# Kernel tuning notes

Hardware: AMD Instinct MI355X
Metric: run time of the kernel (lower is better)

Reference implementation:

```python
import jax, jax.numpy as jnp
import numpy as np

B, C, H, W = 2, 3, 256, 256
K_STEPS = 50
RHO = 0.5
SIGMA_INIT = float(0.5 / np.sqrt(2.0 * C))  # sigma_init == tau_init = 0.5/sqrt(C*2)


def nabla(x):
    # forward finite differences, zero at last row/col. x: [B,C,H,W] -> [B,C,2,H,W]
    dh = jnp.pad(x[:, :, 1:, :] - x[:, :, :-1, :], ((0, 0), (0, 0), (0, 1), (0, 0)))
    dw = jnp.pad(x[:, :, :, 1:] - x[:, :, :, :-1], ((0, 0), (0, 0), (0, 0), (0, 1)))
    return jnp.stack([dh, dw], axis=2)


def nablaT(u):
    # adjoint of nabla (negative divergence). u: [B,C,2,H,W] -> [B,C,H,W]
    v0, v1 = u[:, :, 0], u[:, :, 1]
    out = jnp.zeros(v0.shape, v0.dtype)
    out = out.at[:, :, 1:, :].add(v0[:, :, :-1, :]).at[:, :, :-1, :].add(-v0[:, :, :-1, :])
    out = out.at[:, :, :, 1:].add(v1[:, :, :, :-1]).at[:, :, :, :-1].add(-v1[:, :, :, :-1])
    return out


def l12_prox_conjugate(v, lamb):
    # Moreau: prox_{sigma*(lamb*f)*}(v) = v - sigma*prox_{(lamb/sigma) f}(v/sigma)
    # which for L12 reduces to projection onto the lamb-ball per group.
    # groups: l2 over axes (1,-2,-1) = (C,H,W), one group per (B, F).
    norm = jnp.sqrt(jnp.sum(v * v, axis=(1, 3, 4), keepdims=True))
    scale = lamb / jnp.maximum(norm, lamb)  # == min(1, lamb/norm), safe at 0
    return v * scale


def l2_prox(z, y, gamma):
    # argmin_u 0.5||u-z||^2 + gamma*0.5||u-y||^2  (A = identity)
    return (z + gamma * y) / (1.0 + gamma)


def setup_inputs() -> dict:
    key = jax.random.key(0)
    y = jax.random.normal(key, (B, C, H, W), dtype=jnp.float32)
    lambd = jnp.float32(-1.0)  # learnable scalar log-regularization weight
    return {"y": y, "lambd": lambd}


def reference(y, lambd):
    elambda = jnp.exp(lambd)
    # set_init: A_dagger = identity
    x0 = y
    xt0 = jnp.zeros_like(x0)
    u0 = nabla(x0)

    def step(carry, _):
        x, xt, u, sigma, tau = carry
        u_next = l12_prox_conjugate(u + sigma * nabla(xt), elambda)
        x_next = l2_prox(x - tau * nablaT(u_next), y, tau)
        chi = 1.0 / jnp.sqrt(1.0 + 2.0 * RHO * tau)
        tau_next = tau * chi
        sigma_next = sigma / chi
        xt_next = (1.0 + chi) * x_next - chi * x
        return (x_next, xt_next, u_next, sigma_next, tau_next), None

    init = (x0, xt0, u0, jnp.float32(SIGMA_INIT), jnp.float32(SIGMA_INIT))
    (x, xt, u, _, _), _ = jax.lax.scan(step, init, None, length=K_STEPS)
    return (x, xt, u)
```

## Files before the change

kernel.cpp:

```cpp
#include <hip/hip_runtime.h>
#include <math.h>

constexpr int Cc = 3, Hh = 256;
constexpr int NX = 393216;
constexpr int R = 8;
constexpr int NBLK = 192;
constexpr int KSTEPS = 50;
constexpr int ROWQ = 128;
constexpr int BROWS = 12;
constexpr int SLOTQ = NBLK * BROWS * ROWQ;

using u64 = unsigned long long;
constexpr u64 SENT = 0x8000000080000000ull;

__device__ __forceinline__ float4 ld4(const float* p, int i) { return ((const float4*)p)[i]; }
__device__ __forceinline__ void st4(float* p, int i, float4 v) { ((float4*)p)[i] = v; }
__device__ __forceinline__ float4 mk4(float a, float b, float c, float d) { return make_float4(a, b, c, d); }
__device__ __forceinline__ u64 ldq(const u64* p) {
    return __hip_atomic_load(p, __ATOMIC_RELAXED, __HIP_MEMORY_SCOPE_AGENT);
}
__device__ __forceinline__ void stq(u64* p, u64 v) {
    __hip_atomic_store(p, v, __ATOMIC_RELAXED, __HIP_MEMORY_SCOPE_AGENT);
}
__device__ __forceinline__ void pub4(u64* w, float4 v) {
    union { float f[2]; u64 q; } a, b;
    a.f[0] = v.x; a.f[1] = v.y; b.f[0] = v.z; b.f[1] = v.w;
    stq(w, a.q); stq(w + 1, b.q);
}
__device__ __forceinline__ float4 unp(u64 lo, u64 hi) {
    union { u64 q; float f[2]; } a, b; a.q = lo; b.q = hi;
    return make_float4(a.f[0], a.f[1], b.f[0], b.f[1]);
}
__device__ __forceinline__ float4 col3(float4 P, float4 A, float4 B, float a, float b) {
    return mk4(fmaf(a, A.x, fmaf(b, B.x, P.x)), fmaf(a, A.y, fmaf(b, B.y, P.y)),
               fmaf(a, A.z, fmaf(b, B.z, P.z)), fmaf(a, A.w, fmaf(b, B.w, P.w)));
}
__device__ __forceinline__ float4 f4sub(float4 a, float4 b) {
    return mk4(a.x - b.x, a.y - b.y, a.z - b.z, a.w - b.w);
}
__device__ __forceinline__ float4 f4s(float4 a, float s) {
    return mk4(a.x * s, a.y * s, a.z * s, a.w * s);
}
__device__ __forceinline__ float4 f4fma(float s, float4 a, float4 b) {
    return mk4(fmaf(s, a.x, b.x), fmaf(s, a.y, b.y), fmaf(s, a.z, b.z), fmaf(s, a.w, b.w));
}
__device__ __forceinline__ float4 nth(float4 vm, bool up, float4 v0x, bool dn) {
    return mk4((up ? vm.x : 0.f) - (dn ? v0x.x : 0.f), (up ? vm.y : 0.f) - (dn ? v0x.y : 0.f),
               (up ? vm.z : 0.f) - (dn ? v0x.z : 0.f), (up ? vm.w : 0.f) - (dn ? v0x.w : 0.f));
}
__device__ __forceinline__ float4 ntw(float4 v1x, int c4) {
    float ul = __shfl_up(v1x.w, 1, 64);
    return mk4(((c4 > 0) ? ul : 0.f) - v1x.x, v1x.x - v1x.y, v1x.y - v1x.z,
               v1x.z - ((c4 < 63) ? v1x.w : 0.f));
}
__device__ __forceinline__ float4 gradw(float4 t, int c4) {
    float xn = __shfl_down(t.x, 1, 64);
    return mk4(t.y - t.x, t.z - t.y, t.w - t.z, (c4 < 63) ? (xn - t.w) : 0.f);
}
__device__ __forceinline__ void barld() {
    asm volatile("s_waitcnt lgkmcnt(0)" ::: "memory");
    __builtin_amdgcn_sched_barrier(0);
    __builtin_amdgcn_s_barrier();
    __builtin_amdgcn_sched_barrier(0);
}

__global__ void init_ws(u64* h0, u64* h1, u64* h2, u64* parts) {
    int i = blockIdx.x * 256 + threadIdx.x;
    if (i < SLOTQ) { h0[i] = SENT; h1[i] = SENT; h2[i] = SENT; }
    if (i < (KSTEPS + 1) * NBLK) parts[i] = SENT;
}

__global__ void __launch_bounds__(512, 1) cp_persist(
    const float* __restrict__ y, const float* __restrict__ lambd,
    float* __restrict__ xout, float* __restrict__ xtout, float* __restrict__ uout,
    u64* __restrict__ h0, u64* __restrict__ h1, u64* __restrict__ h2,
    u64* __restrict__ parts)
{
    __shared__ float sv0[8 * 256];
    __shared__ float sxtP[9 * 256];
    __shared__ float sxtA[9 * 256];
    __shared__ float sxtB[9 * 256];
    __shared__ float2 pw[8];

    const int tid = threadIdx.x, blk = blockIdx.x;
    const int bc = blk >> 5, tile = blk & 31, r0 = tile * R;
    const int c4 = tid & 63, trow = tid >> 6;
    const int b = (bc >= Cc) ? 1 : 0;
    const float lamb = expf(lambd[0]);
    const int gh = r0 + trow;
    const int j4 = bc * 16384 + gh * 64 + c4;

    float4 yv, xcur, v0c, v1c;
    float4 xpP, xpA, xpB, p0P, p0A, p0B, p1P, p1A, p1B;
    float4 yh = mk4(0, 0, 0, 0), vmtop = yh, v0h = yh, v1h = yh, xoh = yh;

    float tau = 0.20412414523193150818f;
    float sig = tau;
    float chi = 0.f, sigs = 0.f;
    float alpha = 0.f, beta = 0.f;

    auto slotp = [&](int r) -> u64* { return (r == 0) ? h0 : ((r == 1) ? h1 : h2); };

    auto wavesum2 = [&](float& a, float& bb) {
        #pragma unroll
        for (int m = 1; m < 64; m <<= 1) { a += __shfl_xor(a, m, 64); bb += __shfl_xor(bb, m, 64); }
    };

    auto pollscale = [&](int s) {
        const u64* pb = parts + (size_t)s * NBLK + b * 96;
        const int i1 = 64 + (c4 & 31);
        u64 q0, q1;
        for (;;) {
            q0 = ldq(pb + c4);
            q1 = ldq(pb + i1);
            if (__all((q0 != SENT) && (q1 != SENT))) break;
            __builtin_amdgcn_s_sleep(1);
        }
        asm volatile("" ::: "memory");
        union { u64 q; float f[2]; } a;
        a.q = q0;
        float g0 = a.f[0], g1 = a.f[1];
        a.q = q1;
        if (c4 < 32) { g0 += a.f[0]; g1 += a.f[1]; }
        wavesum2(g0, g1);
        alpha = lamb / fmaxf(sqrtf(g0), lamb);
        beta  = lamb / fmaxf(sqrtf(g1), lamb);
    };

    auto wavenorm = [&]() {
        float pa0 = v0c.x*v0c.x + v0c.y*v0c.y + v0c.z*v0c.z + v0c.w*v0c.w;
        float pa1 = v1c.x*v1c.x + v1c.y*v1c.y + v1c.z*v1c.z + v1c.w*v1c.w;
        wavesum2(pa0, pa1);
        if (c4 == 0) pw[trow] = make_float2(pa0, pa1);
    };
    auto pubparts = [&](int s) {
        if (tid == 0) {
            float q0 = 0.f, q1 = 0.f;
            #pragma unroll
            for (int w = 0; w < 8; ++w) { q0 += pw[w].x; q1 += pw[w].y; }
            union { float f[2]; u64 q; } pk; pk.f[0] = q0; pk.f[1] = q1;
            stq(parts + (size_t)s * NBLK + blk, pk.q);
        }
    };

    auto expand = [&](u64* hb, bool pub) {
        const float inv = 1.f / (1.f + tau);
        const float tin = tau * inv;
        const float opc = 1.f + chi;
        float4 xtP, xtA, xtB;
        {
            float4 vm = (trow > 0) ? ((float4*)(sv0 + (trow - 1) * 256))[c4] : vmtop;
            float4 NT0 = nth(vm, gh > 0, v0c, gh < Hh - 1);
            float4 NT1 = ntw(v1c, c4);
            float4 BASE = f4s(f4fma(tau, yv, xcur), inv);
            float4 xA = f4s(NT0, -tin);
            float4 xB = f4s(NT1, -tin);
            xpP = BASE; xpA = xA; xpB = xB;
            xtP = f4fma(-chi, xcur, f4s(BASE, opc));
            xtA = f4s(xA, opc);
            xtB = f4s(xB, opc);
            if (trow >= 1) {
                ((float4*)(sxtP + trow * 256))[c4] = xtP;
                ((float4*)(sxtA + trow * 256))[c4] = xtA;
                ((float4*)(sxtB + trow * 256))[c4] = xtB;
            }
            if (pub && trow == 0) {
                u64* rbase = hb + ((size_t)blk * BROWS) * ROWQ;
                pub4(rbase +  9 * ROWQ + 2 * c4, BASE);
                pub4(rbase + 10 * ROWQ + 2 * c4, xA);
                pub4(rbase + 11 * ROWQ + 2 * c4, xB);
            }
        }
        if (trow == 0 && tile < 31) {
            float4 vmh = ((float4*)(sv0 + 7 * 256))[c4];
            float4 NT0h = nth(vmh, true, v0h, true);
            float4 NT1h = ntw(v1h, c4);
            float4 BASEh = f4s(f4fma(tau, yh, xoh), inv);
            float4 xAh = f4s(NT0h, -tin);
            float4 xBh = f4s(NT1h, -tin);
            ((float4*)(sxtP + 8 * 256))[c4] = f4fma(-chi, xoh, f4s(BASEh, opc));
            ((float4*)(sxtA + 8 * 256))[c4] = f4s(xAh, opc);
            ((float4*)(sxtB + 8 * 256))[c4] = f4s(xBh, opc);
        }
        barld();
        {
            float4 dhP = mk4(0, 0, 0, 0), dhA = dhP, dhB = dhP;
            if (gh < Hh - 1) {
                dhP = f4sub(((float4*)(sxtP + (trow + 1) * 256))[c4], xtP);
                dhA = f4sub(((float4*)(sxtA + (trow + 1) * 256))[c4], xtA);
                dhB = f4sub(((float4*)(sxtB + (trow + 1) * 256))[c4], xtB);
            }
            float4 dwP = gradw(xtP, c4);
            float4 dwA = gradw(xtA, c4);
            float4 dwB = gradw(xtB, c4);
            p0P = f4s(dhP, sigs);
            p0A = f4fma(sigs, dhA, v0c);
            p0B = f4s(dhB, sigs);
            p1P = f4s(dwP, sigs);
            p1A = f4s(dwA, sigs);
            p1B = f4fma(sigs, dwB, v1c);
            if (pub) {
                u64* rbase = hb + ((size_t)blk * BROWS) * ROWQ;
                if (trow == 0) {
                    pub4(rbase + 3 * ROWQ + 2 * c4, p0P);
                    pub4(rbase + 4 * ROWQ + 2 * c4, p0A);
                    pub4(rbase + 5 * ROWQ + 2 * c4, p0B);
                    pub4(rbase + 6 * ROWQ + 2 * c4, p1P);
                    pub4(rbase + 7 * ROWQ + 2 * c4, p1A);
                    pub4(rbase + 8 * ROWQ + 2 * c4, p1B);
                }
                if (trow == 7) {
                    pub4(rbase + 0 * ROWQ + 2 * c4, p0P);
                    pub4(rbase + 1 * ROWQ + 2 * c4, p0A);
                    pub4(rbase + 2 * ROWQ + 2 * c4, p0B);
                }
            }
        }
        barld();
    };

    {
        yv = ld4(y, j4);
        xcur = yv;
        float4 dh = mk4(0, 0, 0, 0);
        if (gh < Hh - 1) dh = f4sub(ld4(y, j4 + 64), yv);
        v0c = dh;
        v1c = gradw(yv, c4);
        ((float4*)(sv0 + trow * 256))[c4] = v0c;
        if (trow == 0) {
            if (tile < 31) {
                const int j4h = bc * 16384 + (r0 + 8) * 64 + c4;
                yh = ld4(y, j4h);
                v0h = f4sub(ld4(y, j4h + 64), yh);
                v1h = gradw(yh, c4);
                xoh = yh;
            }
            if (tile > 0) {
                float4 ym = ld4(y, bc * 16384 + (r0 - 1) * 64 + c4);
                vmtop = f4sub(yv, ym);
            }
        }
        wavenorm();
        barld();
        pubparts(1);
        chi = 1.f / sqrtf(1.f + tau);
        sigs = sig / chi;
        expand(slotp(0), true);
        tau *= chi; sig = sigs;
    }

    for (int s = 1; s < KSTEPS; ++s) {
        pollscale(s);
        chi = 1.f / sqrtf(1.f + tau);
        sigs = sig / chi;

        xcur = col3(xpP, xpA, xpB, alpha, beta);
        v0c  = col3(p0P, p0A, p0B, alpha, beta);
        v1c  = col3(p1P, p1A, p1B, alpha, beta);
        ((float4*)(sv0 + trow * 256))[c4] = v0c;

        u64* hbp = slotp((s - 1) % 3);
        if (trow == 0) {
            if (tile > 0) {
                const u64* ra = hbp + ((size_t)(blk - 1) * BROWS) * ROWQ + 2 * c4;
                u64 a0, a1, a2, a3, a4, a5;
                for (;;) {
                    a0 = ldq(ra);            a1 = ldq(ra + 1);
                    a2 = ldq(ra + ROWQ);     a3 = ldq(ra + ROWQ + 1);
                    a4 = ldq(ra + 2 * ROWQ); a5 = ldq(ra + 2 * ROWQ + 1);
                    if (__all((a0 != SENT) && (a1 != SENT) && (a2 != SENT) &&
                              (a3 != SENT) && (a4 != SENT) && (a5 != SENT))) break;
                    __builtin_amdgcn_s_sleep(1);
                }
                vmtop = col3(unp(a0, a1), unp(a2, a3), unp(a4, a5), alpha, beta);
            }
            if (tile < 31) {
                const u64* rb = hbp + ((size_t)(blk + 1) * BROWS) * ROWQ + 2 * c4;
                u64 b0, b1, b2, b3, b4, b5, b6, b7, b8, b9, b10, b11, b12, b13, b14, b15, b16, b17;
                for (;;) {
                    b0  = ldq(rb + 3 * ROWQ);  b1  = ldq(rb + 3 * ROWQ + 1);
                    b2  = ldq(rb + 4 * ROWQ);  b3  = ldq(rb + 4 * ROWQ + 1);
                    b4  = ldq(rb + 5 * ROWQ);  b5  = ldq(rb + 5 * ROWQ + 1);
                    b6  = ldq(rb + 6 * ROWQ);  b7  = ldq(rb + 6 * ROWQ + 1);
                    b8  = ldq(rb + 7 * ROWQ);  b9  = ldq(rb + 7 * ROWQ + 1);
                    b10 = ldq(rb + 8 * ROWQ);  b11 = ldq(rb + 8 * ROWQ + 1);
                    b12 = ldq(rb + 9 * ROWQ);  b13 = ldq(rb + 9 * ROWQ + 1);
                    b14 = ldq(rb + 10 * ROWQ); b15 = ldq(rb + 10 * ROWQ + 1);
                    b16 = ldq(rb + 11 * ROWQ); b17 = ldq(rb + 11 * ROWQ + 1);
                    bool ok = (b0 != SENT) && (b1 != SENT) && (b2 != SENT) && (b3 != SENT) &&
                              (b4 != SENT) && (b5 != SENT) && (b6 != SENT) && (b7 != SENT) &&
                              (b8 != SENT) && (b9 != SENT) && (b10 != SENT) && (b11 != SENT) &&
                              (b12 != SENT) && (b13 != SENT) && (b14 != SENT) && (b15 != SENT) &&
                              (b16 != SENT) && (b17 != SENT);
                    if (__all(ok)) break;
                    __builtin_amdgcn_s_sleep(1);
                }
                v0h = col3(unp(b0, b1),   unp(b2, b3),   unp(b4, b5),   alpha, beta);
                v1h = col3(unp(b6, b7),   unp(b8, b9),   unp(b10, b11), alpha, beta);
                xoh = col3(unp(b12, b13), unp(b14, b15), unp(b16, b17), alpha, beta);
            }
        }
        asm volatile("" ::: "memory");

        if (s <= 47) {
            u64* rb2 = slotp((s + 1) % 3) + ((size_t)blk * BROWS) * ROWQ;
            if (trow == 0) {
                #pragma unroll
                for (int r = 3; r < 12; ++r) {
                    stq(rb2 + r * ROWQ + 2 * c4, SENT);
                    stq(rb2 + r * ROWQ + 2 * c4 + 1, SENT);
                }
            } else if (trow == 7) {
                #pragma unroll
                for (int r = 0; r < 3; ++r) {
                    stq(rb2 + r * ROWQ + 2 * c4, SENT);
                    stq(rb2 + r * ROWQ + 2 * c4 + 1, SENT);
                }
            }
        }
        wavenorm();
        barld();
        pubparts(s + 1);
        expand(slotp(s % 3), s < KSTEPS - 1);
        tau *= chi; sig = sigs;
    }

    pollscale(KSTEPS);
    const float opc = 1.f + chi;
    const int iv4 = bc * 32768 + gh * 64 + c4;
    float4 xf_ = col3(xpP, xpA, xpB, alpha, beta);
    float4 xtf = f4fma(-chi, xcur, f4s(xf_, opc));
    st4(xout, j4, xf_);
    st4(xtout, j4, xtf);
    st4(uout, iv4, f4s(v0c, alpha));
    st4(uout, iv4 + 16384, f4s(v1c, beta));
}

extern "C" void kernel_launch(void* const* d_in, const int* in_sizes, int n_in,
                              void* d_out, int out_size, void* d_ws, size_t ws_size,
                              hipStream_t stream) {
    (void)in_sizes; (void)n_in; (void)out_size; (void)ws_size;
    const float* y     = (const float*)d_in[0];
    const float* lambd = (const float*)d_in[1];
    float* xout  = (float*)d_out;
    float* xtout = xout + NX;
    float* uout  = xout + 2 * NX;

    u64* h0 = (u64*)d_out;
    u64* h1 = h0 + SLOTQ;
    u64* h2 = (u64*)d_ws;
    u64* parts = h2 + SLOTQ;

    init_ws<<<SLOTQ / 256, 256, 0, stream>>>(h0, h1, h2, parts);
    cp_persist<<<NBLK, 512, 0, stream>>>(y, lambd, xout, xtout, uout, h0, h1, h2, parts);
}
```

Baseline: 208.5 us.

## Publish per-wave norm partials and recompute neighbor rows to cut block barriers

Result: slower. 306.2 us (+46.9%).

```diff
diff --git a/kernel.cpp b/kernel.cpp
--- a/kernel.cpp
+++ b/kernel.cpp
@@ -9,6 +9,7 @@
 constexpr int ROWQ = 128;
 constexpr int BROWS = 12;
 constexpr int SLOTQ = NBLK * BROWS * ROWQ;
+constexpr int WPS = NBLK * 8;
 
 using u64 = unsigned long long;
 constexpr u64 SENT = 0x8000000080000000ull;
@@ -67,7 +68,7 @@
 __global__ void init_ws(u64* h0, u64* h1, u64* h2, u64* parts) {
     int i = blockIdx.x * 256 + threadIdx.x;
     if (i < SLOTQ) { h0[i] = SENT; h1[i] = SENT; h2[i] = SENT; }
-    if (i < (KSTEPS + 1) * NBLK) parts[i] = SENT;
+    if (i < (KSTEPS + 1) * WPS) parts[i] = SENT;
 }
 
 __global__ void __launch_bounds__(512, 1) cp_persist(
@@ -76,11 +77,8 @@
     u64* __restrict__ h0, u64* __restrict__ h1, u64* __restrict__ h2,
     u64* __restrict__ parts)
 {
-    __shared__ float sv0[8 * 256];
-    __shared__ float sxtP[9 * 256];
-    __shared__ float sxtA[9 * 256];
-    __shared__ float sxtB[9 * 256];
-    __shared__ float2 pw[8];
+    __shared__ float PCS[8][9][256];
+    __shared__ float sG[2];
 
     const int tid = threadIdx.x, blk = blockIdx.x;
     const int bc = blk >> 5, tile = blk & 31, r0 = tile * R;
@@ -89,180 +87,118 @@
     const float lamb = expf(lambd[0]);
     const int gh = r0 + trow;
     const int j4 = bc * 16384 + gh * 64 + c4;
-
-    float4 yv, xcur, v0c, v1c;
-    float4 xpP, xpA, xpB, p0P, p0A, p0B, p1P, p1A, p1B;
-    float4 yh = mk4(0, 0, 0, 0), vmtop = yh, v0h = yh, v1h = yh, xoh = yh;
-
-    float tau = 0.20412414523193150818f;
-    float sig = tau;
-    float chi = 0.f, sigs = 0.f;
-    float alpha = 0.f, beta = 0.f;
+    const bool have2 = (gh < Hh - 1);
+    const bool dn2 = (gh < Hh - 2);
+
+    float4 pc[9];
+    float4 xcur, x2, v0c, v0c2, v1c, v1c2, vm;
+    float4 yv, yv2;
+    float tau = 0.20412414523193150818f, sig = tau, chi, sigs;
 
     auto slotp = [&](int r) -> u64* { return (r == 0) ? h0 : ((r == 1) ? h1 : h2); };
-
+    auto ldsF = [&](int row, int f) -> float4& { return ((float4*)PCS[row][f])[c4]; };
     auto wavesum2 = [&](float& a, float& bb) {
         #pragma unroll
         for (int m = 1; m < 64; m <<= 1) { a += __shfl_xor(a, m, 64); bb += __shfl_xor(bb, m, 64); }
     };
-
-    auto pollscale = [&](int s) {
-        const u64* pb = parts + (size_t)s * NBLK + b * 96;
-        const int i1 = 64 + (c4 & 31);
-        u64 q0, q1;
+    auto pollparts = [&](int s, float& g0, float& g1) {
+        const u64* pb = parts + (size_t)s * WPS + b * 768 + c4 * 12;
+        u64 t[12];
         for (;;) {
-            q0 = ldq(pb + c4);
-            q1 = ldq(pb + i1);
-            if (__all((q0 != SENT) && (q1 != SENT))) break;
+            #pragma unroll
+            for (int i = 0; i < 12; ++i) t[i] = ldq(pb + i);
+            bool ok = true;
+            #pragma unroll
+            for (int i = 0; i < 12; ++i) ok = ok && (t[i] != SENT);
+            if (__all(ok)) break;
             __builtin_amdgcn_s_sleep(1);
         }
         asm volatile("" ::: "memory");
-        union { u64 q; float f[2]; } a;
-        a.q = q0;
-        float g0 = a.f[0], g1 = a.f[1];
-        a.q = q1;
-        if (c4 < 32) { g0 += a.f[0]; g1 += a.f[1]; }
+        g0 = 0.f; g1 = 0.f;
+        #pragma unroll
+        for (int i = 0; i < 12; ++i) { union { u64 q; float f[2]; } a; a.q = t[i]; g0 += a.f[0]; g1 += a.f[1]; }
         wavesum2(g0, g1);
-        alpha = lamb / fmaxf(sqrtf(g0), lamb);
-        beta  = lamb / fmaxf(sqrtf(g1), lamb);
     };
-
-    auto wavenorm = [&]() {
+    auto normpub = [&](int sidx) {
         float pa0 = v0c.x*v0c.x + v0c.y*v0c.y + v0c.z*v0c.z + v0c.w*v0c.w;
         float pa1 = v1c.x*v1c.x + v1c.y*v1c.y + v1c.z*v1c.z + v1c.w*v1c.w;
         wavesum2(pa0, pa1);
-        if (c4 == 0) pw[trow] = make_float2(pa0, pa1);
+        if (c4 == 0) {
+            union { float f[2]; u64 q; } pk; pk.f[0] = pa0; pk.f[1] = pa1;
+            stq(parts + (size_t)sidx * WPS + blk * 8 + trow, pk.q);
+        }
     };
-    auto pubparts = [&](int s) {
-        if (tid == 0) {
-            float q0 = 0.f, q1 = 0.f;
-            #pragma unroll
-            for (int w = 0; w < 8; ++w) { q0 += pw[w].x; q1 += pw[w].y; }
-            union { float f[2]; u64 q; } pk; pk.f[0] = q0; pk.f[1] = q1;
-            stq(parts + (size_t)s * NBLK + blk, pk.q);
-        }
-    };
-
-    auto expand = [&](u64* hb, bool pub) {
-        const float inv = 1.f / (1.f + tau);
-        const float tin = tau * inv;
-        const float opc = 1.f + chi;
-        float4 xtP, xtA, xtB;
-        {
-            float4 vm = (trow > 0) ? ((float4*)(sv0 + (trow - 1) * 256))[c4] : vmtop;
-            float4 NT0 = nth(vm, gh > 0, v0c, gh < Hh - 1);
-            float4 NT1 = ntw(v1c, c4);
-            float4 BASE = f4s(f4fma(tau, yv, xcur), inv);
-            float4 xA = f4s(NT0, -tin);
-            float4 xB = f4s(NT1, -tin);
-            xpP = BASE; xpA = xA; xpB = xB;
-            xtP = f4fma(-chi, xcur, f4s(BASE, opc));
-            xtA = f4s(xA, opc);
-            xtB = f4s(xB, opc);
-            if (trow >= 1) {
-                ((float4*)(sxtP + trow * 256))[c4] = xtP;
-                ((float4*)(sxtA + trow * 256))[c4] = xtA;
-                ((float4*)(sxtB + trow * 256))[c4] = xtB;
+    auto expandF = [&](int slot, bool pub) {
+        const float inv = 1.f / (1.f + tau), tin = tau * inv, opc = 1.f + chi;
+        float4 NT0 = nth(vm, gh > 0, v0c, have2);
+        float4 NT1 = ntw(v1c, c4);
+        float4 BASE = f4s(f4fma(tau, yv, xcur), inv);
+        float4 xA = f4s(NT0, -tin), xB = f4s(NT1, -tin);
+        float4 xtP = f4fma(-chi, xcur, f4s(BASE, opc)), xtA = f4s(xA, opc), xtB = f4s(xB, opc);
+        float4 dhP = mk4(0, 0, 0, 0), dhA = dhP, dhB = dhP;
+        if (have2) {
+            float4 NT0b = nth(v0c, true, v0c2, dn2);
+            float4 NT1b = ntw(v1c2, c4);
+            float4 BASEb = f4s(f4fma(tau, yv2, x2), inv);
+            float4 xAb = f4s(NT0b, -tin), xBb = f4s(NT1b, -tin);
+            dhP = f4sub(f4fma(-chi, x2, f4s(BASEb, opc)), xtP);
+            dhA = f4sub(f4s(xAb, opc), xtA);
+            dhB = f4sub(f4s(xBb, opc), xtB);
+        }
+        float4 dwP = gradw(xtP, c4), dwA = gradw(xtA, c4), dwB = gradw(xtB, c4);
+        pc[0] = BASE; pc[1] = xA; pc[2] = xB;
+        pc[3] = f4s(dhP, sigs); pc[4] = f4fma(sigs, dhA, v0c); pc[5] = f4s(dhB, sigs);
+        pc[6] = f4s(dwP, sigs); pc[7] = f4s(dwA, sigs); pc[8] = f4fma(sigs, dwB, v1c);
+        #pragma unroll
+        for (int f = 0; f < 9; ++f) ldsF(trow, f) = pc[f];
+        if (pub) {
+            u64* rbase = slotp(slot) + ((size_t)blk * BROWS) * ROWQ;
+            if (trow == 0) {
+                #pragma unroll
+                for (int f = 0; f < 6; ++f) pub4(rbase + (3 + f) * ROWQ + 2 * c4, pc[3 + f]);
+                #pragma unroll
+                for (int f = 0; f < 3; ++f) pub4(rbase + (9 + f) * ROWQ + 2 * c4, pc[f]);
+            } else if (trow == 7) {
+                #pragma unroll
+                for (int f = 0; f < 3; ++f) pub4(rbase + f * ROWQ + 2 * c4, pc[3 + f]);
             }
-            if (pub && trow == 0) {
-                u64* rbase = hb + ((size_t)blk * BROWS) * ROWQ;
-                pub4(rbase +  9 * ROWQ + 2 * c4, BASE);
-                pub4(rbase + 10 * ROWQ + 2 * c4, xA);
-                pub4(rbase + 11 * ROWQ + 2 * c4, xB);
-            }
-        }
-        if (trow == 0 && tile < 31) {
-            float4 vmh = ((float4*)(sv0 + 7 * 256))[c4];
-            float4 NT0h = nth(vmh, true, v0h, true);
-            float4 NT1h = ntw(v1h, c4);
-            float4 BASEh = f4s(f4fma(tau, yh, xoh), inv);
-            float4 xAh = f4s(NT0h, -tin);
-            float4 xBh = f4s(NT1h, -tin);
-            ((float4*)(sxtP + 8 * 256))[c4] = f4fma(-chi, xoh, f4s(BASEh, opc));
-            ((float4*)(sxtA + 8 * 256))[c4] = f4s(xAh, opc);
-            ((float4*)(sxtB + 8 * 256))[c4] = f4s(xBh, opc);
-        }
-        barld();
-        {
-            float4 dhP = mk4(0, 0, 0, 0), dhA = dhP, dhB = dhP;
-            if (gh < Hh - 1) {
-                dhP = f4sub(((float4*)(sxtP + (trow + 1) * 256))[c4], xtP);
-                dhA = f4sub(((float4*)(sxtA + (trow + 1) * 256))[c4], xtA);
-                dhB = f4sub(((float4*)(sxtB + (trow + 1) * 256))[c4], xtB);
-            }
-            float4 dwP = gradw(xtP, c4);
-            float4 dwA = gradw(xtA, c4);
-            float4 dwB = gradw(xtB, c4);
-            p0P = f4s(dhP, sigs);
-            p0A = f4fma(sigs, dhA, v0c);
-            p0B = f4s(dhB, sigs);
-            p1P = f4s(dwP, sigs);
-            p1A = f4s(dwA, sigs);
-            p1B = f4fma(sigs, dwB, v1c);
-            if (pub) {
-                u64* rbase = hb + ((size_t)blk * BROWS) * ROWQ;
-                if (trow == 0) {
-                    pub4(rbase + 3 * ROWQ + 2 * c4, p0P);
-                    pub4(rbase + 4 * ROWQ + 2 * c4, p0A);
-                    pub4(rbase + 5 * ROWQ + 2 * c4, p0B);
-                    pub4(rbase + 6 * ROWQ + 2 * c4, p1P);
-                    pub4(rbase + 7 * ROWQ + 2 * c4, p1A);
-                    pub4(rbase + 8 * ROWQ + 2 * c4, p1B);
-                }
-                if (trow == 7) {
-                    pub4(rbase + 0 * ROWQ + 2 * c4, p0P);
-                    pub4(rbase + 1 * ROWQ + 2 * c4, p0A);
-                    pub4(rbase + 2 * ROWQ + 2 * c4, p0B);
-                }
-            }
-        }
-        barld();
+        }
     };
 
     {
         yv = ld4(y, j4);
-        xcur = yv;
-        float4 dh = mk4(0, 0, 0, 0);
-        if (gh < Hh - 1) dh = f4sub(ld4(y, j4 + 64), yv);
-        v0c = dh;
+        yv2 = have2 ? ld4(y, j4 + 64) : mk4(0, 0, 0, 0);
+        xcur = yv; x2 = yv2;
+        v0c = have2 ? f4sub(yv2, yv) : mk4(0, 0, 0, 0);
         v1c = gradw(yv, c4);
-        ((float4*)(sv0 + trow * 256))[c4] = v0c;
-        if (trow == 0) {
-            if (tile < 31) {
-                const int j4h = bc * 16384 + (r0 + 8) * 64 + c4;
-                yh = ld4(y, j4h);
-                v0h = f4sub(ld4(y, j4h + 64), yh);
-                v1h = gradw(yh, c4);
-                xoh = yh;
-            }
-            if (tile > 0) {
-                float4 ym = ld4(y, bc * 16384 + (r0 - 1) * 64 + c4);
-                vmtop = f4sub(yv, ym);
-            }
-        }
-        wavenorm();
-        barld();
-        pubparts(1);
+        float4 y3 = dn2 ? ld4(y, j4 + 128) : mk4(0, 0, 0, 0);
+        v0c2 = dn2 ? f4sub(y3, yv2) : mk4(0, 0, 0, 0);
+        v1c2 = gradw(yv2, c4);
+        vm = (gh > 0) ? f4sub(yv, ld4(y, j4 - 64)) : mk4(0, 0, 0, 0);
+        normpub(1);
         chi = 1.f / sqrtf(1.f + tau);
         sigs = sig / chi;
-        expand(slotp(0), true);
+        expandF(0, true);
         tau *= chi; sig = sigs;
+        if (trow == 3) {
+            float g0, g1; pollparts(1, g0, g1);
+            if (c4 == 0) { sG[0] = g0; sG[1] = g1; }
+        }
     }
 
-    for (int s = 1; s < KSTEPS; ++s) {
-        pollscale(s);
+    for (int s = 1; s < KSTEPS - 1; ++s) {
+        barld();
+        float al, be;
+        { float g0 = sG[0], g1 = sG[1];
+          al = lamb / fmaxf(sqrtf(g0), lamb);
+          be = lamb / fmaxf(sqrtf(g1), lamb); }
         chi = 1.f / sqrtf(1.f + tau);
         sigs = sig / chi;
-
-        xcur = col3(xpP, xpA, xpB, alpha, beta);
-        v0c  = col3(p0P, p0A, p0B, alpha, beta);
-        v1c  = col3(p1P, p1A, p1B, alpha, beta);
-        ((float4*)(sv0 + trow * 256))[c4] = v0c;
-
-        u64* hbp = slotp((s - 1) % 3);
+        const int ps = (s - 1) % 3;
+
         if (trow == 0) {
             if (tile > 0) {
-                const u64* ra = hbp + ((size_t)(blk - 1) * BROWS) * ROWQ + 2 * c4;
+                const u64* ra = slotp(ps) + ((size_t)(blk - 1) * BROWS) * ROWQ + 2 * c4;
                 u64 a0, a1, a2, a3, a4, a5;
                 for (;;) {
                     a0 = ldq(ra);            a1 = ldq(ra + 1);
@@ -272,33 +208,24 @@
                               (a3 != SENT) && (a4 != SENT) && (a5 != SENT))) break;
                     __builtin_amdgcn_s_sleep(1);
                 }
-                vmtop = col3(unp(a0, a1), unp(a2, a3), unp(a4, a5), alpha, beta);
+                vm = col3(unp(a0, a1), unp(a2, a3), unp(a4, a5), al, be);
+            } else vm = mk4(0, 0, 0, 0);
+        }
+        if (trow == 7 && tile < 31) {
+            const u64* rb = slotp(ps) + ((size_t)(blk + 1) * BROWS) * ROWQ + 2 * c4;
+            u64 t[18];
+            for (;;) {
+                #pragma unroll
+                for (int i = 0; i < 9; ++i) { t[2 * i] = ldq(rb + (3 + i) * ROWQ); t[2 * i + 1] = ldq(rb + (3 + i) * ROWQ + 1); }
+                bool ok = true;
+                #pragma unroll
+                for (int i = 0; i < 18; ++i) ok = ok && (t[i] != SENT);
+                if (__all(ok)) break;
+                __builtin_amdgcn_s_sleep(1);
             }
-            if (tile < 31) {
-                const u64* rb = hbp + ((size_t)(blk + 1) * BROWS) * ROWQ + 2 * c4;
-                u64 b0, b1, b2, b3, b4, b5, b6, b7, b8, b9, b10, b11, b12, b13, b14, b15, b16, b17;
-                for (;;) {
-                    b0  = ldq(rb + 3 * ROWQ);  b1  = ldq(rb + 3 * ROWQ + 1);
-                    b2  = ldq(rb + 4 * ROWQ);  b3  = ldq(rb + 4 * ROWQ + 1);
-                    b4  = ldq(rb + 5 * ROWQ);  b5  = ldq(rb + 5 * ROWQ + 1);
-                    b6  = ldq(rb + 6 * ROWQ);  b7  = ldq(rb + 6 * ROWQ + 1);
-                    b8  = ldq(rb + 7 * ROWQ);  b9  = ldq(rb + 7 * ROWQ + 1);
-                    b10 = ldq(rb + 8 * ROWQ);  b11 = ldq(rb + 8 * ROWQ + 1);
-                    b12 = ldq(rb + 9 * ROWQ);  b13 = ldq(rb + 9 * ROWQ + 1);
-                    b14 = ldq(rb + 10 * ROWQ); b15 = ldq(rb + 10 * ROWQ + 1);
-                    b16 = ldq(rb + 11 * ROWQ); b17 = ldq(rb + 11 * ROWQ + 1);
-                    bool ok = (b0 != SENT) && (b1 != SENT) && (b2 != SENT) && (b3 != SENT) &&
-                              (b4 != SENT) && (b5 != SENT) && (b6 != SENT) && (b7 != SENT) &&
-                              (b8 != SENT) && (b9 != SENT) && (b10 != SENT) && (b11 != SENT) &&
-                              (b12 != SENT) && (b13 != SENT) && (b14 != SENT) && (b15 != SENT) &&
-                              (b16 != SENT) && (b17 != SENT);
-                    if (__all(ok)) break;
-                    __builtin_amdgcn_s_sleep(1);
-                }
-                v0h = col3(unp(b0, b1),   unp(b2, b3),   unp(b4, b5),   alpha, beta);
-                v1h = col3(unp(b6, b7),   unp(b8, b9),   unp(b10, b11), alpha, beta);
-                xoh = col3(unp(b12, b13), unp(b14, b15), unp(b16, b17), alpha, beta);
-            }
+            v0c2 = col3(unp(t[0], t[1]),   unp(t[2], t[3]),   unp(t[4], t[5]),   al, be);
+            v1c2 = col3(unp(t[6], t[7]),   unp(t[8], t[9]),   unp(t[10], t[11]), al, be);
+            x2   = col3(unp(t[12], t[13]), unp(t[14], t[15]), unp(t[16], t[17]), al, be);
         }
         asm volatile("" ::: "memory");
 
@@ -306,34 +233,80 @@
             u64* rb2 = slotp((s + 1) % 3) + ((size_t)blk * BROWS) * ROWQ;
             if (trow == 0) {
                 #pragma unroll
-                for (int r = 3; r < 12; ++r) {
-                    stq(rb2 + r * ROWQ + 2 * c4, SENT);
-                    stq(rb2 + r * ROWQ + 2 * c4 + 1, SENT);
+                for (int r = 3; r < 12; ++r) { stq(rb2 + r * ROWQ + 2 * c4, SENT); stq(rb2 + r * ROWQ + 2 * c4 + 1, SENT); }
+            } else if (trow == 7) {
+                #pragma unroll
+                for (int r = 0; r < 3; ++r) { stq(rb2 + r * ROWQ + 2 * c4, SENT); stq(rb2 + r * ROWQ + 2 * c4 + 1, SENT); }
+            }
+        }
+
+        if (trow > 0) vm = col3(ldsF(trow - 1, 3), ldsF(trow - 1, 4), ldsF(trow - 1, 5), al, be);
+        xcur = col3(pc[0], pc[1], pc[2], al, be);
+        v0c  = col3(pc[3], pc[4], pc[5], al, be);
+        v1c  = col3(pc[6], pc[7], pc[8], al, be);
+        if (trow < 7) {
+            x2   = col3(ldsF(trow + 1, 0), ldsF(trow + 1, 1), ldsF(trow + 1, 2), al, be);
+            v0c2 = col3(ldsF(trow + 1, 3), ldsF(trow + 1, 4), ldsF(trow + 1, 5), al, be);
+            v1c2 = col3(ldsF(trow + 1, 6), ldsF(trow + 1, 7), ldsF(trow + 1, 8), al, be);
+        }
+        normpub(s + 1);
+        barld();
+        expandF(s % 3, true);
+        tau *= chi; sig = sigs;
+        if (trow == 3) {
+            float g0, g1; pollparts(s + 1, g0, g1);
+            if (c4 == 0) { sG[0] = g0; sG[1] = g1; }
+        }
+    }
+
+    {
+        barld();
+        float al, be;
+        { float g0 = sG[0], g1 = sG[1];
+          al = lamb / fmaxf(sqrtf(g0), lamb);
+          be = lamb / fmaxf(sqrtf(g1), lamb); }
+        chi = 1.f / sqrtf(1.f + tau);
+        const int ps = (KSTEPS - 2) % 3;
+        if (trow == 0) {
+            if (tile > 0) {
+                const u64* ra = slotp(ps) + ((size_t)(blk - 1) * BROWS) * ROWQ + 2 * c4;
+                u64 a0, a1, a2, a3, a4, a5;
+                for (;;) {
+                    a0 = ldq(ra);            a1 = ldq(ra + 1);
+                    a2 = ldq(ra + ROWQ);     a3 = ldq(ra + ROWQ + 1);
+                    a4 = ldq(ra + 2 * ROWQ); a5 = ldq(ra + 2 * ROWQ + 1);
+                    if (__all((a0 != SENT) && (a1 != SENT) && (a2 != SENT) &&
+                              (a3 != SENT) && (a4 != SENT) && (a5 != SENT))) break;
+                    __builtin_amdgcn_s_sleep(1);
                 }
-            } else if (trow == 7) {
-                #pragma unroll
-                for (int r = 0; r < 3; ++r) {
-                    stq(rb2 + r * ROWQ + 2 * c4, SENT);
-                    stq(rb2 + r * ROWQ + 2 * c4 + 1, SENT);
-                }
-            }
-        }
-        wavenorm();
-        barld();
-        pubparts(s + 1);
-        expand(slotp(s % 3), s < KSTEPS - 1);
-        tau *= chi; sig = sigs;
+                vm = col3(unp(a0, a1), unp(a2, a3), unp(a4, a5), al, be);
+            } else vm = mk4(0, 0, 0, 0);
+        }
+        asm volatile("" ::: "memory");
+        if (trow > 0) vm = col3(ldsF(trow - 1, 3), ldsF(trow - 1, 4), ldsF(trow - 1, 5), al, be);
+        xcur = col3(pc[0], pc[1], pc[2], al, be);
+        v0c  = col3(pc[3], pc[4], pc[5], al, be);
+        v1c  = col3(pc[6], pc[7], pc[8], al, be);
+        normpub(KSTEPS);
+
+        const float inv = 1.f / (1.f + tau), tin = tau * inv;
+        float4 NT0 = nth(vm, gh > 0, v0c, have2);
+        float4 NT1 = ntw(v1c, c4);
+        float4 BASE = f4s(f4fma(tau, yv, xcur), inv);
+        float4 xA = f4s(NT0, -tin), xB = f4s(NT1, -tin);
+
+        float g0, g1;
+        pollparts(KSTEPS, g0, g1);
+        const float a50 = lamb / fmaxf(sqrtf(g0), lamb);
+        const float b50 = lamb / fmaxf(sqrtf(g1), lamb);
+        float4 x50 = col3(BASE, xA, xB, a50, b50);
+        float4 xt50 = f4fma(-chi, xcur, f4s(x50, 1.f + chi));
+        const int iv4 = bc * 32768 + gh * 64 + c4;
+        st4(xout, j4, x50);
+        st4(xtout, j4, xt50);
+        st4(uout, iv4, f4s(v0c, a50));
+        st4(uout, iv4 + 16384, f4s(v1c, b50));
     }
-
-    pollscale(KSTEPS);
-    const float opc = 1.f + chi;
-    const int iv4 = bc * 32768 + gh * 64 + c4;
-    float4 xf_ = col3(xpP, xpA, xpB, alpha, beta);
-    float4 xtf = f4fma(-chi, xcur, f4s(xf_, opc));
-    st4(xout, j4, xf_);
-    st4(xtout, j4, xtf);
-    st4(uout, iv4, f4s(v0c, alpha));
-    st4(uout, iv4 + 16384, f4s(v1c, beta));
 }
 
 extern "C" void kernel_launch(void* const* d_in, const int* in_sizes, int n_in,
```

## Compute group norms from quadratic-form partial dots to overlap global norm reduction

Applied to the files above, without the earlier changes.

Result: slower. 342.9 us (+64.5%).

```diff
diff --git a/kernel.cpp b/kernel.cpp
--- a/kernel.cpp
+++ b/kernel.cpp
@@ -9,6 +9,8 @@
 constexpr int ROWQ = 128;
 constexpr int BROWS = 12;
 constexpr int SLOTQ = NBLK * BROWS * ROWQ;
+constexpr int REC1W = NBLK * 8;
+constexpr int QRECW = (KSTEPS - 1) * 6 * NBLK;
 
 using u64 = unsigned long long;
 constexpr u64 SENT = 0x8000000080000000ull;
@@ -57,6 +59,9 @@
     float xn = __shfl_down(t.x, 1, 64);
     return mk4(t.y - t.x, t.z - t.y, t.w - t.z, (c4 < 63) ? (xn - t.w) : 0.f);
 }
+__device__ __forceinline__ float dot4(float4 a, float4 b) {
+    return a.x * b.x + a.y * b.y + a.z * b.z + a.w * b.w;
+}
 __device__ __forceinline__ void barld() {
     asm volatile("s_waitcnt lgkmcnt(0)" ::: "memory");
     __builtin_amdgcn_sched_barrier(0);
@@ -64,23 +69,22 @@
     __builtin_amdgcn_sched_barrier(0);
 }
 
-__global__ void init_ws(u64* h0, u64* h1, u64* h2, u64* parts) {
+__global__ void init_ws(u64* h0, u64* h1, u64* h2, u64* tail) {
     int i = blockIdx.x * 256 + threadIdx.x;
     if (i < SLOTQ) { h0[i] = SENT; h1[i] = SENT; h2[i] = SENT; }
-    if (i < (KSTEPS + 1) * NBLK) parts[i] = SENT;
+    if (i < REC1W + QRECW + NBLK) tail[i] = SENT;
 }
 
 __global__ void __launch_bounds__(512, 1) cp_persist(
     const float* __restrict__ y, const float* __restrict__ lambd,
     float* __restrict__ xout, float* __restrict__ xtout, float* __restrict__ uout,
     u64* __restrict__ h0, u64* __restrict__ h1, u64* __restrict__ h2,
-    u64* __restrict__ parts)
+    u64* __restrict__ rec1, u64* __restrict__ qrec, u64* __restrict__ grec)
 {
     __shared__ float sv0[8 * 256];
-    __shared__ float sxtP[9 * 256];
-    __shared__ float sxtA[9 * 256];
-    __shared__ float sxtB[9 * 256];
-    __shared__ float2 pw[8];
+    __shared__ float sxtP[9 * 256], sxtA[9 * 256], sxtB[9 * 256];
+    __shared__ float qc[8][12];
+    __shared__ float qp[8][2];
 
     const int tid = threadIdx.x, blk = blockIdx.x;
     const int bc = blk >> 5, tile = blk & 31, r0 = tile * R;
@@ -90,141 +94,137 @@
     const int gh = r0 + trow;
     const int j4 = bc * 16384 + gh * 64 + c4;
 
-    float4 yv, xcur, v0c, v1c;
-    float4 xpP, xpA, xpB, p0P, p0A, p0B, p1P, p1A, p1B;
+    float4 yv, xcur, v0c, v1c, pc[9];
     float4 yh = mk4(0, 0, 0, 0), vmtop = yh, v0h = yh, v1h = yh, xoh = yh;
-
-    float tau = 0.20412414523193150818f;
-    float sig = tau;
-    float chi = 0.f, sigs = 0.f;
-    float alpha = 0.f, beta = 0.f;
+    float tau = 0.20412414523193150818f, sig = tau, chi = 0.f, sigs = 0.f;
+    float ap = 0.f, bp = 0.f;
 
     auto slotp = [&](int r) -> u64* { return (r == 0) ? h0 : ((r == 1) ? h1 : h2); };
-
     auto wavesum2 = [&](float& a, float& bb) {
         #pragma unroll
         for (int m = 1; m < 64; m <<= 1) { a += __shfl_xor(a, m, 64); bb += __shfl_xor(bb, m, 64); }
     };
 
-    auto pollscale = [&](int s) {
-        const u64* pb = parts + (size_t)s * NBLK + b * 96;
-        const int i1 = 64 + (c4 & 31);
-        u64 q0, q1;
-        for (;;) {
-            q0 = ldq(pb + c4);
-            q1 = ldq(pb + i1);
-            if (__all((q0 != SENT) && (q1 != SENT))) break;
-            __builtin_amdgcn_s_sleep(1);
-        }
-        asm volatile("" ::: "memory");
-        union { u64 q; float f[2]; } a;
-        a.q = q0;
-        float g0 = a.f[0], g1 = a.f[1];
-        a.q = q1;
-        if (c4 < 32) { g0 += a.f[0]; g1 += a.f[1]; }
-        wavesum2(g0, g1);
-        alpha = lamb / fmaxf(sqrtf(g0), lamb);
-        beta  = lamb / fmaxf(sqrtf(g1), lamb);
-    };
-
-    auto wavenorm = [&]() {
-        float pa0 = v0c.x*v0c.x + v0c.y*v0c.y + v0c.z*v0c.z + v0c.w*v0c.w;
-        float pa1 = v1c.x*v1c.x + v1c.y*v1c.y + v1c.z*v1c.z + v1c.w*v1c.w;
-        wavesum2(pa0, pa1);
-        if (c4 == 0) pw[trow] = make_float2(pa0, pa1);
-    };
-    auto pubparts = [&](int s) {
-        if (tid == 0) {
-            float q0 = 0.f, q1 = 0.f;
-            #pragma unroll
-            for (int w = 0; w < 8; ++w) { q0 += pw[w].x; q1 += pw[w].y; }
-            union { float f[2]; u64 q; } pk; pk.f[0] = q0; pk.f[1] = q1;
-            stq(parts + (size_t)s * NBLK + blk, pk.q);
-        }
-    };
-
     auto expand = [&](u64* hb, bool pub) {
-        const float inv = 1.f / (1.f + tau);
-        const float tin = tau * inv;
-        const float opc = 1.f + chi;
-        float4 xtP, xtA, xtB;
-        {
-            float4 vm = (trow > 0) ? ((float4*)(sv0 + (trow - 1) * 256))[c4] : vmtop;
-            float4 NT0 = nth(vm, gh > 0, v0c, gh < Hh - 1);
-            float4 NT1 = ntw(v1c, c4);
-            float4 BASE = f4s(f4fma(tau, yv, xcur), inv);
-            float4 xA = f4s(NT0, -tin);
-            float4 xB = f4s(NT1, -tin);
-            xpP = BASE; xpA = xA; xpB = xB;
-            xtP = f4fma(-chi, xcur, f4s(BASE, opc));
-            xtA = f4s(xA, opc);
-            xtB = f4s(xB, opc);
-            if (trow >= 1) {
-                ((float4*)(sxtP + trow * 256))[c4] = xtP;
-                ((float4*)(sxtA + trow * 256))[c4] = xtA;
-                ((float4*)(sxtB + trow * 256))[c4] = xtB;
-            }
-            if (pub && trow == 0) {
-                u64* rbase = hb + ((size_t)blk * BROWS) * ROWQ;
-                pub4(rbase +  9 * ROWQ + 2 * c4, BASE);
-                pub4(rbase + 10 * ROWQ + 2 * c4, xA);
-                pub4(rbase + 11 * ROWQ + 2 * c4, xB);
-            }
+        const float inv = 1.f / (1.f + tau), tin = tau * inv, opc = 1.f + chi;
+        float4 vm = (trow > 0) ? ((float4*)(sv0 + (trow - 1) * 256))[c4] : vmtop;
+        float4 NT0 = nth(vm, gh > 0, v0c, gh < Hh - 1);
+        float4 NT1 = ntw(v1c, c4);
+        float4 BASE = f4s(f4fma(tau, yv, xcur), inv);
+        float4 xA = f4s(NT0, -tin), xB = f4s(NT1, -tin);
+        float4 xtP = f4fma(-chi, xcur, f4s(BASE, opc)), xtA = f4s(xA, opc), xtB = f4s(xB, opc);
+        pc[0] = BASE; pc[1] = xA; pc[2] = xB;
+        if (trow >= 1) {
+            ((float4*)(sxtP + trow * 256))[c4] = xtP;
+            ((float4*)(sxtA + trow * 256))[c4] = xtA;
+            ((float4*)(sxtB + trow * 256))[c4] = xtB;
+        }
+        u64* rbase = hb + ((size_t)blk * BROWS) * ROWQ;
+        if (pub && trow == 0) {
+            pub4(rbase +  9 * ROWQ + 2 * c4, BASE);
+            pub4(rbase + 10 * ROWQ + 2 * c4, xA);
+            pub4(rbase + 11 * ROWQ + 2 * c4, xB);
         }
         if (trow == 0 && tile < 31) {
             float4 vmh = ((float4*)(sv0 + 7 * 256))[c4];
             float4 NT0h = nth(vmh, true, v0h, true);
             float4 NT1h = ntw(v1h, c4);
             float4 BASEh = f4s(f4fma(tau, yh, xoh), inv);
-            float4 xAh = f4s(NT0h, -tin);
-            float4 xBh = f4s(NT1h, -tin);
             ((float4*)(sxtP + 8 * 256))[c4] = f4fma(-chi, xoh, f4s(BASEh, opc));
-            ((float4*)(sxtA + 8 * 256))[c4] = f4s(xAh, opc);
-            ((float4*)(sxtB + 8 * 256))[c4] = f4s(xBh, opc);
-        }
-        barld();
-        {
-            float4 dhP = mk4(0, 0, 0, 0), dhA = dhP, dhB = dhP;
-            if (gh < Hh - 1) {
-                dhP = f4sub(((float4*)(sxtP + (trow + 1) * 256))[c4], xtP);
-                dhA = f4sub(((float4*)(sxtA + (trow + 1) * 256))[c4], xtA);
-                dhB = f4sub(((float4*)(sxtB + (trow + 1) * 256))[c4], xtB);
-            }
-            float4 dwP = gradw(xtP, c4);
-            float4 dwA = gradw(xtA, c4);
-            float4 dwB = gradw(xtB, c4);
-            p0P = f4s(dhP, sigs);
-            p0A = f4fma(sigs, dhA, v0c);
-            p0B = f4s(dhB, sigs);
-            p1P = f4s(dwP, sigs);
-            p1A = f4s(dwA, sigs);
-            p1B = f4fma(sigs, dwB, v1c);
-            if (pub) {
-                u64* rbase = hb + ((size_t)blk * BROWS) * ROWQ;
-                if (trow == 0) {
-                    pub4(rbase + 3 * ROWQ + 2 * c4, p0P);
-                    pub4(rbase + 4 * ROWQ + 2 * c4, p0A);
-                    pub4(rbase + 5 * ROWQ + 2 * c4, p0B);
-                    pub4(rbase + 6 * ROWQ + 2 * c4, p1P);
-                    pub4(rbase + 7 * ROWQ + 2 * c4, p1A);
-                    pub4(rbase + 8 * ROWQ + 2 * c4, p1B);
-                }
-                if (trow == 7) {
-                    pub4(rbase + 0 * ROWQ + 2 * c4, p0P);
-                    pub4(rbase + 1 * ROWQ + 2 * c4, p0A);
-                    pub4(rbase + 2 * ROWQ + 2 * c4, p0B);
-                }
-            }
-        }
-        barld();
+            ((float4*)(sxtA + 8 * 256))[c4] = f4s(f4s(NT0h, -tin), opc);
+            ((float4*)(sxtB + 8 * 256))[c4] = f4s(f4s(NT1h, -tin), opc);
+        }
+        barld();
+        float4 dhP = mk4(0, 0, 0, 0), dhA = dhP, dhB = dhP;
+        if (gh < Hh - 1) {
+            dhP = f4sub(((float4*)(sxtP + (trow + 1) * 256))[c4], xtP);
+            dhA = f4sub(((float4*)(sxtA + (trow + 1) * 256))[c4], xtA);
+            dhB = f4sub(((float4*)(sxtB + (trow + 1) * 256))[c4], xtB);
+        }
+        float4 dwP = gradw(xtP, c4), dwA = gradw(xtA, c4), dwB = gradw(xtB, c4);
+        pc[3] = f4s(dhP, sigs); pc[4] = f4fma(sigs, dhA, v0c); pc[5] = f4s(dhB, sigs);
+        pc[6] = f4s(dwP, sigs); pc[7] = f4s(dwA, sigs); pc[8] = f4fma(sigs, dwB, v1c);
+        if (pub) {
+            if (trow == 0) {
+                pub4(rbase + 3 * ROWQ + 2 * c4, pc[3]);
+                pub4(rbase + 4 * ROWQ + 2 * c4, pc[4]);
+                pub4(rbase + 5 * ROWQ + 2 * c4, pc[5]);
+                pub4(rbase + 6 * ROWQ + 2 * c4, pc[6]);
+                pub4(rbase + 7 * ROWQ + 2 * c4, pc[7]);
+                pub4(rbase + 8 * ROWQ + 2 * c4, pc[8]);
+            } else if (trow == 7) {
+                pub4(rbase + 0 * ROWQ + 2 * c4, pc[3]);
+                pub4(rbase + 1 * ROWQ + 2 * c4, pc[4]);
+                pub4(rbase + 2 * ROWQ + 2 * c4, pc[5]);
+            }
+        }
+    };
+
+    auto qdots = [&]() {
+        float d[12];
+        d[0]  = dot4(pc[3], pc[3]); d[1]  = dot4(pc[3], pc[4]);
+        d[2]  = dot4(pc[4], pc[4]); d[3]  = dot4(pc[3], pc[5]);
+        d[4]  = dot4(pc[5], pc[5]); d[5]  = dot4(pc[4], pc[5]);
+        d[6]  = dot4(pc[6], pc[6]); d[7]  = dot4(pc[6], pc[7]);
+        d[8]  = dot4(pc[7], pc[7]); d[9]  = dot4(pc[6], pc[8]);
+        d[10] = dot4(pc[8], pc[8]); d[11] = dot4(pc[7], pc[8]);
+        #pragma unroll
+        for (int i = 0; i < 12; i += 2) wavesum2(d[i], d[i + 1]);
+        if (c4 == 0) {
+            #pragma unroll
+            for (int i = 0; i < 12; ++i) qc[trow][i] = d[i];
+        }
+    };
+    auto recpub = [&](int s) {
+        if (trow == 6 && c4 < 6) {
+            float s0 = 0.f, s1 = 0.f;
+            #pragma unroll
+            for (int w = 0; w < 8; ++w) { s0 += qc[w][2 * c4]; s1 += qc[w][2 * c4 + 1]; }
+            union { float f[2]; u64 q; } pk; pk.f[0] = s0; pk.f[1] = s1;
+            stq(qrec + ((size_t)(s - 2) * 6 + c4) * NBLK + blk, pk.q);
+        }
+    };
+    auto qpoll = [&](int s) {
+        if (trow < 6) {
+            const u64* base = qrec + ((size_t)(s - 2) * 6 + trow) * NBLK + b * 96;
+            const bool two = (c4 < 32);
+            u64 t0, t1 = 0;
+            for (;;) {
+                t0 = ldq(base + c4);
+                bool ok = (t0 != SENT);
+                if (two) { t1 = ldq(base + 64 + c4); ok = ok && (t1 != SENT); }
+                if (__all(ok)) break;
+                __builtin_amdgcn_s_sleep(1);
+            }
+            asm volatile("" ::: "memory");
+            union { u64 q; float f[2]; } a; a.q = t0;
+            float g0 = a.f[0], g1 = a.f[1];
+            if (two) { a.q = t1; g0 += a.f[0]; g1 += a.f[1]; }
+            wavesum2(g0, g1);
+            if (c4 == 0) { qp[trow][0] = g0; qp[trow][1] = g1; }
+        }
+    };
+    auto evalAB = [&](bool classic, float& ao, float& bo) {
+        if (classic) {
+            float n0 = 0.f, n1 = 0.f;
+            #pragma unroll
+            for (int w = 0; w < 8; ++w) { n0 += qp[w][0]; n1 += qp[w][1]; }
+            ao = lamb / fmaxf(sqrtf(n0), lamb);
+            bo = lamb / fmaxf(sqrtf(n1), lamb);
+        } else {
+            float n0 = qp[0][0] + ap * ap * qp[1][0] + bp * bp * qp[2][0]
+                     + 2.f * (ap * qp[0][1] + bp * qp[1][1] + ap * bp * qp[2][1]);
+            float n1 = qp[3][0] + ap * ap * qp[4][0] + bp * bp * qp[5][0]
+                     + 2.f * (ap * qp[3][1] + bp * qp[4][1] + ap * bp * qp[5][1]);
+            ao = lamb / fmaxf(sqrtf(n0), lamb);
+            bo = lamb / fmaxf(sqrtf(n1), lamb);
+        }
     };
 
     {
         yv = ld4(y, j4);
         xcur = yv;
-        float4 dh = mk4(0, 0, 0, 0);
-        if (gh < Hh - 1) dh = f4sub(ld4(y, j4 + 64), yv);
-        v0c = dh;
+        v0c = (gh < Hh - 1) ? f4sub(ld4(y, j4 + 64), yv) : mk4(0, 0, 0, 0);
         v1c = gradw(yv, c4);
         ((float4*)(sv0 + trow * 256))[c4] = v0c;
         if (trow == 0) {
@@ -240,26 +240,67 @@
                 vmtop = f4sub(yv, ym);
             }
         }
-        wavenorm();
-        barld();
-        pubparts(1);
+        float pa0 = dot4(v0c, v0c), pa1 = dot4(v1c, v1c);
+        wavesum2(pa0, pa1);
+        if (c4 == 0) {
+            union { float f[2]; u64 q; } pk; pk.f[0] = pa0; pk.f[1] = pa1;
+            stq(rec1 + blk * 8 + trow, pk.q);
+        }
         chi = 1.f / sqrtf(1.f + tau);
         sigs = sig / chi;
+        barld();
         expand(slotp(0), true);
+        qdots();
+        barld();
+        recpub(2);
+        {
+            const u64* base = rec1 + b * 768 + trow * 96;
+            const bool two = (c4 < 32);
+            u64 t0, t1 = 0;
+            for (;;) {
+                t0 = ldq(base + c4);
+                bool ok = (t0 != SENT);
+                if (two) { t1 = ldq(base + 64 + c4); ok = ok && (t1 != SENT); }
+                if (__all(ok)) break;
+                __builtin_amdgcn_s_sleep(1);
+            }
+            asm volatile("" ::: "memory");
+            union { u64 q; float f[2]; } a; a.q = t0;
+            float g0 = a.f[0], g1 = a.f[1];
+            if (two) { a.q = t1; g0 += a.f[0]; g1 += a.f[1]; }
+            wavesum2(g0, g1);
+            if (c4 == 0) { qp[trow][0] = g0; qp[trow][1] = g1; }
+        }
         tau *= chi; sig = sigs;
     }
 
-    for (int s = 1; s < KSTEPS; ++s) {
-        pollscale(s);
+    for (int n = 1; n <= KSTEPS - 2; ++n) {
+        barld();
+        float al, be;
+        evalAB(n == 1, al, be);
         chi = 1.f / sqrtf(1.f + tau);
         sigs = sig / chi;
-
-        xcur = col3(xpP, xpA, xpB, alpha, beta);
-        v0c  = col3(p0P, p0A, p0B, alpha, beta);
-        v1c  = col3(p1P, p1A, p1B, alpha, beta);
+        {
+            u64* rb2 = slotp(n % 3) + ((size_t)blk * BROWS) * ROWQ;
+            if (trow == 0) {
+                #pragma unroll
+                for (int r = 3; r < 12; ++r) {
+                    stq(rb2 + r * ROWQ + 2 * c4, SENT);
+                    stq(rb2 + r * ROWQ + 2 * c4 + 1, SENT);
+                }
+            } else if (trow == 7) {
+                #pragma unroll
+                for (int r = 0; r < 3; ++r) {
+                    stq(rb2 + r * ROWQ + 2 * c4, SENT);
+                    stq(rb2 + r * ROWQ + 2 * c4 + 1, SENT);
+                }
+            }
+        }
+        xcur = col3(pc[0], pc[1], pc[2], al, be);
+        v0c  = col3(pc[3], pc[4], pc[5], al, be);
+        v1c  = col3(pc[6], pc[7], pc[8], al, be);
         ((float4*)(sv0 + trow * 256))[c4] = v0c;
-
-        u64* hbp = slotp((s - 1) % 3);
+        u64* hbp = slotp((n - 1) % 3);
         if (trow == 0) {
             if (tile > 0) {
                 const u64* ra = hbp + ((size_t)(blk - 1) * BROWS) * ROWQ + 2 * c4;
@@ -272,8 +313,8 @@
                               (a3 != SENT) && (a4 != SENT) && (a5 != SENT))) break;
                     __builtin_amdgcn_s_sleep(1);
                 }
-                vmtop = col3(unp(a0, a1), unp(a2, a3), unp(a4, a5), alpha, beta);
-            }
+                vmtop = col3(unp(a0, a1), unp(a2, a3), unp(a4, a5), al, be);
+            } else vmtop = mk4(0, 0, 0, 0);
             if (tile < 31) {
                 const u64* rb = hbp + ((size_t)(blk + 1) * BROWS) * ROWQ + 2 * c4;
                 u64 b0, b1, b2, b3, b4, b5, b6, b7, b8, b9, b10, b11, b12, b13, b14, b15, b16, b17;
@@ -295,45 +336,78 @@
                     if (__all(ok)) break;
                     __builtin_amdgcn_s_sleep(1);
                 }
-                v0h = col3(unp(b0, b1),   unp(b2, b3),   unp(b4, b5),   alpha, beta);
-                v1h = col3(unp(b6, b7),   unp(b8, b9),   unp(b10, b11), alpha, beta);
-                xoh = col3(unp(b12, b13), unp(b14, b15), unp(b16, b17), alpha, beta);
+                v0h = col3(unp(b0, b1),   unp(b2, b3),   unp(b4, b5),   al, be);
+                v1h = col3(unp(b6, b7),   unp(b8, b9),   unp(b10, b11), al, be);
+                xoh = col3(unp(b12, b13), unp(b14, b15), unp(b16, b17), al, be);
             }
         }
         asm volatile("" ::: "memory");
-
-        if (s <= 47) {
-            u64* rb2 = slotp((s + 1) % 3) + ((size_t)blk * BROWS) * ROWQ;
-            if (trow == 0) {
-                #pragma unroll
-                for (int r = 3; r < 12; ++r) {
-                    stq(rb2 + r * ROWQ + 2 * c4, SENT);
-                    stq(rb2 + r * ROWQ + 2 * c4 + 1, SENT);
-                }
-            } else if (trow == 7) {
-                #pragma unroll
-                for (int r = 0; r < 3; ++r) {
-                    stq(rb2 + r * ROWQ + 2 * c4, SENT);
-                    stq(rb2 + r * ROWQ + 2 * c4 + 1, SENT);
-                }
-            }
-        }
-        wavenorm();
-        barld();
-        pubparts(s + 1);
-        expand(slotp(s % 3), s < KSTEPS - 1);
+        barld();
+        expand(slotp(n % 3), true);
+        qdots();
+        barld();
+        recpub(n + 2);
+        qpoll(n + 1);
+        ap = al; bp = be;
         tau *= chi; sig = sigs;
     }
 
-    pollscale(KSTEPS);
-    const float opc = 1.f + chi;
-    const int iv4 = bc * 32768 + gh * 64 + c4;
-    float4 xf_ = col3(xpP, xpA, xpB, alpha, beta);
-    float4 xtf = f4fma(-chi, xcur, f4s(xf_, opc));
-    st4(xout, j4, xf_);
-    st4(xtout, j4, xtf);
-    st4(uout, iv4, f4s(v0c, alpha));
-    st4(uout, iv4 + 16384, f4s(v1c, beta));
+    {
+        barld();
+        float al, be;
+        evalAB(false, al, be);
+        chi = 1.f / sqrtf(1.f + tau);
+        xcur = col3(pc[0], pc[1], pc[2], al, be);
+        v0c  = col3(pc[3], pc[4], pc[5], al, be);
+        v1c  = col3(pc[6], pc[7], pc[8], al, be);
+        ((float4*)(sv0 + trow * 256))[c4] = v0c;
+        if (trow == 0) {
+            if (tile > 0) {
+                const u64* ra = slotp(0) + ((size_t)(blk - 1) * BROWS) * ROWQ + 2 * c4;
+                u64 a0, a1, a2, a3, a4, a5;
+                for (;;) {
+                    a0 = ldq(ra);            a1 = ldq(ra + 1);
+                    a2 = ldq(ra + ROWQ);     a3 = ldq(ra + ROWQ + 1);
+                    a4 = ldq(ra + 2 * ROWQ); a5 = ldq(ra + 2 * ROWQ + 1);
+                    if (__all((a0 != SENT) && (a1 != SENT) && (a2 != SENT) &&
+                              (a3 != SENT) && (a4 != SENT) && (a5 != SENT))) break;
+                    __builtin_amdgcn_s_sleep(1);
+                }
+                vmtop = col3(unp(a0, a1), unp(a2, a3), unp(a4, a5), al, be);
+            } else vmtop = mk4(0, 0, 0, 0);
+        }
+        asm volatile("" ::: "memory");
+        barld();
+        const float inv = 1.f / (1.f + tau), tin = tau * inv;
+        float4 vm = (trow > 0) ? ((float4*)(sv0 + (trow - 1) * 256))[c4] : vmtop;
+        float4 NT0 = nth(vm, gh > 0, v0c, gh < Hh - 1);
+        float4 NT1 = ntw(v1c, c4);
+        float4 BASE = f4s(f4fma(tau, yv, xcur), inv);
+        float4 xA = f4s(NT0, -tin), xB = f4s(NT1, -tin);
+        if (tid == 0) stq(grec + blk, 0ull);
+        qpoll(KSTEPS);
+        ap = al; bp = be;
+        barld();
+        float a50, b50;
+        evalAB(false, a50, b50);
+        {
+            const u64* g = grec + c4 * 3;
+            u64 g0, g1, g2;
+            for (;;) {
+                g0 = ldq(g); g1 = ldq(g + 1); g2 = ldq(g + 2);
+                if (__all((g0 != SENT) && (g1 != SENT) && (g2 != SENT))) break;
+                __builtin_amdgcn_s_sleep(1);
+            }
+            asm volatile("" ::: "memory");
+        }
+        float4 x50 = col3(BASE, xA, xB, a50, b50);
+        float4 xt50 = f4fma(-chi, xcur, f4s(x50, 1.f + chi));
+        const int iv4 = bc * 32768 + gh * 64 + c4;
+        st4(xout, j4, x50);
+        st4(xtout, j4, xt50);
+        st4(uout, iv4, f4s(v0c, a50));
+        st4(uout, iv4 + 16384, f4s(v1c, b50));
+    }
 }
 
 extern "C" void kernel_launch(void* const* d_in, const int* in_sizes, int n_in,
@@ -349,8 +423,12 @@
     u64* h0 = (u64*)d_out;
     u64* h1 = h0 + SLOTQ;
     u64* h2 = (u64*)d_ws;
-    u64* parts = h2 + SLOTQ;
-
-    init_ws<<<SLOTQ / 256, 256, 0, stream>>>(h0, h1, h2, parts);
-    cp_persist<<<NBLK, 512, 0, stream>>>(y, lambd, xout, xtout, uout, h0, h1, h2, parts);
-}
+    u64* tail = h2 + SLOTQ;
+    u64* rec1 = tail;
+    u64* qrec = rec1 + REC1W;
+    u64* grec = qrec + QRECW;
+
+    init_ws<<<SLOTQ / 256, 256, 0, stream>>>(h0, h1, h2, tail);
+    cp_persist<<<NBLK, 512, 0, stream>>>(y, lambd, xout, xtout, uout,
+                                         h0, h1, h2, rec1, qrec, grec);
+}
```
